# Kernel optimization log

Hardware: AMD Instinct MI355X
Metric: run time of the kernel (lower is better)

## Reference

```python
import jax, jax.numpy as jnp
import numpy as np

OUTPUT_DIM = 512
INPUT_DIM = 64
BATCH = 131072


def setup_inputs() -> dict:
    key = jax.random.key(0)
    k1, k2, k3, k4 = jax.random.split(key, 4)
    D = INPUT_DIM + OUTPUT_DIM
    X = jax.random.normal(k1, (BATCH, OUTPUT_DIM), dtype=jnp.float32)
    c = jax.random.normal(k2, (BATCH, INPUT_DIM), dtype=jnp.float32)
    PA = jax.random.normal(k3, (OUTPUT_DIM, D), dtype=jnp.float32) * 0.05
    PB = jax.random.normal(k4, (OUTPUT_DIM, D), dtype=jnp.float32) * 0.05
    return {"X": X, "c": c, "PA": PA, "PB": PB}


def reference(X, c, PA, PB):
    # x = cat(c, X) : [B, D] with D = INPUT_DIM + OUTPUT_DIM
    x = jnp.concatenate([c, X], axis=1)
    D = INPUT_DIM + OUTPUT_DIM
    mask = (jnp.arange(D)[None, :] < (INPUT_DIM + jnp.arange(OUTPUT_DIM))[:, None]).astype(x.dtype)
    A = x @ (PA * mask).T  # [B, OUTPUT_DIM], A[:, i] = pa[i] @ x[:, :INPUT_DIM+i]
    Bv = x @ (PB * mask).T  # [B, OUTPUT_DIM]
    z = X * jnp.exp(A) + Bv  # [B, OUTPUT_DIM]
    log_det = jnp.sum(A, axis=1)  # [B]
    return z, log_det
```

## Files before the change

### kernel.cpp

```cpp
#include <hip/hip_runtime.h>
#include <hip/hip_bf16.h>
#include <stdint.h>

#define N_OUT 512
#define N_IN 64
#define D_TOT 576
#define BM 64
#define ROW_BYTES (D_TOT * 2)
#define NWAVES 8

typedef __attribute__((ext_vector_type(8))) short short8_t;
typedef __attribute__((ext_vector_type(4))) float f32x4;
typedef unsigned short u16;

__device__ __forceinline__ u16 f2bf(float f) {
    __hip_bfloat16 h = __float2bfloat16(f);
    return *reinterpret_cast<u16*>(&h);
}
__device__ __forceinline__ float bf2f(u16 u) {
    union { uint32_t u; float f; } v;
    v.u = ((uint32_t)u) << 16;
    return v.f;
}

__global__ void prep_weights_kernel(const float* __restrict__ PA,
                                    const float* __restrict__ PB,
                                    u16* __restrict__ WA,
                                    u16* __restrict__ WB) {
    const int col = blockIdx.x;
    const int lim = N_IN + col;
    const float* pa = PA + (size_t)col * D_TOT;
    const float* pb = PB + (size_t)col * D_TOT;
    for (int k = threadIdx.x; k < D_TOT; k += blockDim.x) {
        int kk = k >> 5, lg = (k >> 3) & 3, j = k & 7;
        size_t dst = ((size_t)(kk * 4 + lg) * N_OUT + col) * 8 + j;
        bool valid = (k < lim);
        WA[dst] = valid ? f2bf(pa[k]) : (u16)0;
        WB[dst] = valid ? f2bf(pb[k]) : (u16)0;
    }
}

__global__ __launch_bounds__(512, 2)
void maf_main_kernel(const float* __restrict__ X,
                     const float* __restrict__ Cc,
                     const u16* __restrict__ WA,
                     const u16* __restrict__ WB,
                     float* __restrict__ Z,
                     float* __restrict__ LD) {
    extern __shared__ char smem[];
    char* xt = smem;
    float* ldsum = (float*)(smem + BM * ROW_BYTES);

    const int tid = threadIdx.x;
    const int r0 = blockIdx.x * BM;

    {
        int row = tid >> 3, cc = tid & 7;
        const float* src = Cc + (size_t)(r0 + row) * N_IN + cc * 8;
        f32x4 v0 = *(const f32x4*)src;
        f32x4 v1 = *(const f32x4*)(src + 4);
        short8_t p;
        p[0] = (short)f2bf(v0[0]); p[1] = (short)f2bf(v0[1]);
        p[2] = (short)f2bf(v0[2]); p[3] = (short)f2bf(v0[3]);
        p[4] = (short)f2bf(v1[0]); p[5] = (short)f2bf(v1[1]);
        p[6] = (short)f2bf(v1[2]); p[7] = (short)f2bf(v1[3]);
        int addr = (row * ROW_BYTES + cc * 16) ^ ((row & 7) << 4);
        *(short8_t*)(xt + addr) = p;
    }
    #pragma unroll
    for (int i = 0; i < 8; ++i) {
        int id = tid + i * 512;
        int row = id >> 6, xc = id & 63;
        const float* src = X + (size_t)(r0 + row) * N_OUT + xc * 8;
        f32x4 v0 = *(const f32x4*)src;
        f32x4 v1 = *(const f32x4*)(src + 4);
        short8_t p;
        p[0] = (short)f2bf(v0[0]); p[1] = (short)f2bf(v0[1]);
        p[2] = (short)f2bf(v0[2]); p[3] = (short)f2bf(v0[3]);
        p[4] = (short)f2bf(v1[0]); p[5] = (short)f2bf(v1[1]);
        p[6] = (short)f2bf(v1[2]); p[7] = (short)f2bf(v1[3]);
        int addr = (row * ROW_BYTES + (8 + xc) * 16) ^ ((row & 7) << 4);
        *(short8_t*)(xt + addr) = p;
    }
    __syncthreads();

    const int wid = tid >> 6;
    const int lane = tid & 63;
    const int lr = lane & 15;
    const int lg = lane >> 4;

    float part[4][4];
    #pragma unroll
    for (int m = 0; m < 4; ++m)
        #pragma unroll
        for (int j = 0; j < 4; ++j) part[m][j] = 0.0f;

    const int groups[2] = { wid, 15 - wid };

    #pragma unroll
    for (int gi = 0; gi < 2; ++gi) {
        const int g = groups[gi];
        const int c0 = g << 5;
        const int ksteps = 3 + g;

        f32x4 accA[4][2], accB[4][2];
        #pragma unroll
        for (int m = 0; m < 4; ++m)
            #pragma unroll
            for (int n = 0; n < 2; ++n) {
                accA[m][n] = (f32x4)(0.0f);
                accB[m][n] = (f32x4)(0.0f);
            }

        #pragma unroll 3
        for (int kk = 0; kk < ksteps; ++kk) {
            const int kb = kk * 64 + lg * 16;
            short8_t a[4];
            #pragma unroll
            for (int m = 0; m < 4; ++m) {
                int row = (m << 4) + lr;
                int addr = (row * ROW_BYTES + kb) ^ ((row & 7) << 4);
                a[m] = *(const short8_t*)(xt + addr);
            }
            short8_t ba[2], bb[2];
            const size_t wbase = (size_t)((kk << 2) + lg) * N_OUT + c0 + lr;
            #pragma unroll
            for (int n = 0; n < 2; ++n) {
                size_t off = (wbase + (n << 4)) * 8;
                ba[n] = *(const short8_t*)(WA + off);
                bb[n] = *(const short8_t*)(WB + off);
            }
            #pragma unroll
            for (int m = 0; m < 4; ++m) {
                #pragma unroll
                for (int n = 0; n < 2; ++n) {
                    accA[m][n] = __builtin_amdgcn_mfma_f32_16x16x32_bf16(a[m], ba[n], accA[m][n], 0, 0, 0);
                    accB[m][n] = __builtin_amdgcn_mfma_f32_16x16x32_bf16(a[m], bb[n], accB[m][n], 0, 0, 0);
                }
            }
        }

        #pragma unroll
        for (int m = 0; m < 4; ++m) {
            #pragma unroll
            for (int n = 0; n < 2; ++n) {
                int col = c0 + (n << 4) + lr;
                #pragma unroll
                for (int j = 0; j < 4; ++j) {
                    int row = (m << 4) + (lg << 2) + j;
                    float Av = accA[m][n][j];
                    float Bv = accB[m][n][j];
                    int xaddr = (row * ROW_BYTES + (N_IN + col) * 2) ^ ((row & 7) << 4);
                    float Xf = bf2f(*(const u16*)(xt + xaddr));
                    Z[(size_t)(r0 + row) * N_OUT + col] = Xf * __expf(Av) + Bv;
                    part[m][j] += Av;
                }
            }
        }
    }

    #pragma unroll
    for (int m = 0; m < 4; ++m) {
        #pragma unroll
        for (int j = 0; j < 4; ++j) {
            float v = part[m][j];
            v += __shfl_xor(v, 1);
            v += __shfl_xor(v, 2);
            v += __shfl_xor(v, 4);
            v += __shfl_xor(v, 8);
            if (lr == 0) ldsum[(wid << 6) + (m << 4) + (lg << 2) + j] = v;
        }
    }
    __syncthreads();
    if (tid < 64) {
        float s = 0.0f;
        #pragma unroll
        for (int w = 0; w < NWAVES; ++w) s += ldsum[(w << 6) + tid];
        LD[(size_t)r0 + tid] = s;
    }
}

extern "C" void kernel_launch(void* const* d_in, const int* in_sizes, int n_in,
                              void* d_out, int out_size, void* d_ws, size_t ws_size,
                              hipStream_t stream) {
    const float* X  = (const float*)d_in[0];
    const float* Cc = (const float*)d_in[1];
    const float* PA = (const float*)d_in[2];
    const float* PB = (const float*)d_in[3];

    u16* WA = (u16*)d_ws;
    u16* WB = WA + (size_t)N_OUT * D_TOT;

    float* Z  = (float*)d_out;
    const size_t batch = (size_t)in_sizes[0] / N_OUT;
    float* LD = Z + batch * N_OUT;

    prep_weights_kernel<<<N_OUT, 256, 0, stream>>>(PA, PB, WA, WB);

    const size_t lds_bytes = (size_t)BM * ROW_BYTES + NWAVES * 64 * sizeof(float);
    (void)hipFuncSetAttribute((const void*)maf_main_kernel,
                              hipFuncAttributeMaxDynamicSharedMemorySize,
                              (int)lds_bytes);
    const int grid = (int)(batch / BM);
    maf_main_kernel<<<grid, 512, lds_bytes, stream>>>(X, Cc, WA, WB, Z, LD);
}
```

Baseline: 234.3 us.

## Split output columns across blocks and pipeline weights and activations through LDS

Each row block is now split across two workgroups by output-column half, so a block only walks the K range its causal mask needs. Weight tiles are double-buffered in LDS via global_load_lds, and activation slices are streamed in per k-step alongside the MFMAs. Before, each wave read its weights directly from global memory and all activations were loaded before any compute. Partial log-det sums go to a workspace and are merged by an extra small kernel. The cost is a barrier every k-step, a 141 KB LDS footprint that allows only one block per CU, reading X twice across the two column halves, and one more launch.

```diff
diff --git a/kernel.cpp b/kernel.cpp
--- a/kernel.cpp
+++ b/kernel.cpp
@@ -6,10 +6,17 @@
 #define N_IN 64
 #define D_TOT 576
 #define BM 64
+#define BN 256
 #define ROW_BYTES (D_TOT * 2)
-#define NWAVES 8
+#define BATCH 131072
+
+#define WOFF 0
+#define XOFF 65536
+#define SOFF 139264
+#define LDS_TOTAL 141312
 
 typedef __attribute__((ext_vector_type(8))) short short8_t;
+typedef __attribute__((ext_vector_type(4))) short short4_t;
 typedef __attribute__((ext_vector_type(4))) float f32x4;
 typedef unsigned short u16;
 
@@ -40,125 +47,170 @@
     }
 }
 
-__global__ __launch_bounds__(512, 2)
+__global__ void ld_merge_kernel(const float* __restrict__ PS,
+                                float* __restrict__ LD) {
+    int i = blockIdx.x * 256 + threadIdx.x;
+    LD[i] = PS[i] + PS[BATCH + i];
+}
+
+__global__ __launch_bounds__(512)
 void maf_main_kernel(const float* __restrict__ X,
                      const float* __restrict__ Cc,
                      const u16* __restrict__ WA,
                      const u16* __restrict__ WB,
                      float* __restrict__ Z,
-                     float* __restrict__ LD) {
+                     float* __restrict__ PS) {
     extern __shared__ char smem[];
-    char* xt = smem;
-    float* ldsum = (float*)(smem + BM * ROW_BYTES);
+    char* wlds = smem + WOFF;
+    char* xt   = smem + XOFF;
+    float* ldsum = (float*)(smem + SOFF);
 
     const int tid = threadIdx.x;
-    const int r0 = blockIdx.x * BM;
-
-    {
-        int row = tid >> 3, cc = tid & 7;
-        const float* src = Cc + (size_t)(r0 + row) * N_IN + cc * 8;
-        f32x4 v0 = *(const f32x4*)src;
-        f32x4 v1 = *(const f32x4*)(src + 4);
-        short8_t p;
-        p[0] = (short)f2bf(v0[0]); p[1] = (short)f2bf(v0[1]);
-        p[2] = (short)f2bf(v0[2]); p[3] = (short)f2bf(v0[3]);
-        p[4] = (short)f2bf(v1[0]); p[5] = (short)f2bf(v1[1]);
-        p[6] = (short)f2bf(v1[2]); p[7] = (short)f2bf(v1[3]);
-        int addr = (row * ROW_BYTES + cc * 16) ^ ((row & 7) << 4);
-        *(short8_t*)(xt + addr) = p;
-    }
-    #pragma unroll
-    for (int i = 0; i < 8; ++i) {
-        int id = tid + i * 512;
-        int row = id >> 6, xc = id & 63;
-        const float* src = X + (size_t)(r0 + row) * N_OUT + xc * 8;
-        f32x4 v0 = *(const f32x4*)src;
-        f32x4 v1 = *(const f32x4*)(src + 4);
-        short8_t p;
-        p[0] = (short)f2bf(v0[0]); p[1] = (short)f2bf(v0[1]);
-        p[2] = (short)f2bf(v0[2]); p[3] = (short)f2bf(v0[3]);
-        p[4] = (short)f2bf(v1[0]); p[5] = (short)f2bf(v1[1]);
-        p[6] = (short)f2bf(v1[2]); p[7] = (short)f2bf(v1[3]);
-        int addr = (row * ROW_BYTES + (8 + xc) * 16) ^ ((row & 7) << 4);
-        *(short8_t*)(xt + addr) = p;
-    }
-    __syncthreads();
-
-    const int wid = tid >> 6;
+    const int bid = blockIdx.x;
+    const int cb  = bid & 1;
+    const int rb  = bid >> 1;
+    const int r0  = rb * BM;
+    const int cbase = cb * BN;
+
+    const int wid  = tid >> 6;
     const int lane = tid & 63;
     const int lr = lane & 15;
     const int lg = lane >> 4;
 
-    float part[4][4];
-    #pragma unroll
-    for (int m = 0; m < 4; ++m)
-        #pragma unroll
-        for (int j = 0; j < 4; ++j) part[m][j] = 0.0f;
-
-    const int groups[2] = { wid, 15 - wid };
-
-    #pragma unroll
-    for (int gi = 0; gi < 2; ++gi) {
-        const int g = groups[gi];
-        const int c0 = g << 5;
-        const int ksteps = 3 + g;
-
-        f32x4 accA[4][2], accB[4][2];
-        #pragma unroll
-        for (int m = 0; m < 4; ++m)
+    const int T0 = (cb << 4) + wid;
+    const int T1 = (cb << 4) + 15 - wid;
+    const int ks0 = (111 + 16 * T0) >> 5;
+    const int ks1 = (111 + 16 * T1) >> 5;
+    const int kmax = 10 + 8 * cb;
+
+    const int xrow = tid >> 3, xq = tid & 7;
+
+    {
+        int kb = xq * 4;
+        f32x4 v = __builtin_nontemporal_load(
+            (const f32x4*)(Cc + (size_t)(r0 + xrow) * N_IN + kb));
+        short4_t p;
+        p[0] = (short)f2bf(v[0]); p[1] = (short)f2bf(v[1]);
+        p[2] = (short)f2bf(v[2]); p[3] = (short)f2bf(v[3]);
+        int addr = (xrow * ROW_BYTES + kb * 2) ^ ((xrow & 7) << 4);
+        *(short4_t*)(xt + addr) = p;
+    }
+    #pragma unroll
+    for (int i = 0; i < 4; ++i) {
+        int f = i * 512 + tid;
+        int mat = f >> 10, q = f & 1023;
+        int lg2 = q >> 8, col = q & 255;
+        const u16* g = (mat ? WB : WA) + ((size_t)lg2 * N_OUT + cbase + col) * 8;
+        char* l = wlds + f * 16;
+        __builtin_amdgcn_global_load_lds(
+            (const __attribute__((address_space(1))) uint32_t*)g,
+            (__attribute__((address_space(3))) uint32_t*)l, 16, 0, 0);
+    }
+    __syncthreads();
+
+    f32x4 aE0[4], aV0[4], aE1[4], aV1[4];
+    #pragma unroll
+    for (int m = 0; m < 4; ++m) {
+        aE0[m] = (f32x4)(0.0f); aV0[m] = (f32x4)(0.0f);
+        aE1[m] = (f32x4)(0.0f); aV1[m] = (f32x4)(0.0f);
+    }
+
+    const int cl0 = ((T0 & 15) << 4) + lr;
+    const int cl1 = ((T1 & 15) << 4) + lr;
+
+    int buf = 0;
+    for (int kk = 0; kk < kmax; ++kk) {
+        const int s = kk + 1;
+        f32x4 xv;
+        if (s < kmax) {
+            int kb = s * 32 + xq * 4;
+            const float* src = (s < 2)
+                ? (Cc + (size_t)(r0 + xrow) * N_IN + kb)
+                : (X + (size_t)(r0 + xrow) * N_OUT + (kb - 64));
+            xv = __builtin_nontemporal_load((const f32x4*)src);
+        }
+        if (s < kmax) {
             #pragma unroll
-            for (int n = 0; n < 2; ++n) {
-                accA[m][n] = (f32x4)(0.0f);
-                accB[m][n] = (f32x4)(0.0f);
-            }
-
-        #pragma unroll 3
-        for (int kk = 0; kk < ksteps; ++kk) {
-            const int kb = kk * 64 + lg * 16;
-            short8_t a[4];
+            for (int i = 0; i < 4; ++i) {
+                int f = i * 512 + tid;
+                int mat = f >> 10, q = f & 1023;
+                int lg2 = q >> 8, col = q & 255;
+                const u16* g = (mat ? WB : WA)
+                    + ((size_t)((s << 2) + lg2) * N_OUT + cbase + col) * 8;
+                char* l = wlds + (buf ^ 1) * 32768 + f * 16;
+                __builtin_amdgcn_global_load_lds(
+                    (const __attribute__((address_space(1))) uint32_t*)g,
+                    (__attribute__((address_space(3))) uint32_t*)l, 16, 0, 0);
+            }
+        }
+        const char* wb_ = wlds + buf * 32768;
+        short8_t a[4];
+        #pragma unroll
+        for (int m = 0; m < 4; ++m) {
+            int row = (m << 4) + lr;
+            int addr = (row * ROW_BYTES + kk * 64 + lg * 16) ^ ((row & 7) << 4);
+            a[m] = *(const short8_t*)(xt + addr);
+        }
+        if (kk < ks0) {
+            short8_t we = *(const short8_t*)(wb_ + ((lg << 8) + cl0) * 16);
+            short8_t wv = *(const short8_t*)(wb_ + 16384 + ((lg << 8) + cl0) * 16);
             #pragma unroll
             for (int m = 0; m < 4; ++m) {
-                int row = (m << 4) + lr;
-                int addr = (row * ROW_BYTES + kb) ^ ((row & 7) << 4);
-                a[m] = *(const short8_t*)(xt + addr);
-            }
-            short8_t ba[2], bb[2];
-            const size_t wbase = (size_t)((kk << 2) + lg) * N_OUT + c0 + lr;
-            #pragma unroll
-            for (int n = 0; n < 2; ++n) {
-                size_t off = (wbase + (n << 4)) * 8;
-                ba[n] = *(const short8_t*)(WA + off);
-                bb[n] = *(const short8_t*)(WB + off);
-            }
+                aE0[m] = __builtin_amdgcn_mfma_f32_16x16x32_bf16(a[m], we, aE0[m], 0, 0, 0);
+                aV0[m] = __builtin_amdgcn_mfma_f32_16x16x32_bf16(a[m], wv, aV0[m], 0, 0, 0);
+            }
+        }
+        if (kk < ks1) {
+            short8_t we = *(const short8_t*)(wb_ + ((lg << 8) + cl1) * 16);
+            short8_t wv = *(const short8_t*)(wb_ + 16384 + ((lg << 8) + cl1) * 16);
             #pragma unroll
             for (int m = 0; m < 4; ++m) {
-                #pragma unroll
-                for (int n = 0; n < 2; ++n) {
-                    accA[m][n] = __builtin_amdgcn_mfma_f32_16x16x32_bf16(a[m], ba[n], accA[m][n], 0, 0, 0);
-                    accB[m][n] = __builtin_amdgcn_mfma_f32_16x16x32_bf16(a[m], bb[n], accB[m][n], 0, 0, 0);
-                }
-            }
-        }
-
-        #pragma unroll
-        for (int m = 0; m < 4; ++m) {
-            #pragma unroll
-            for (int n = 0; n < 2; ++n) {
-                int col = c0 + (n << 4) + lr;
-                #pragma unroll
-                for (int j = 0; j < 4; ++j) {
-                    int row = (m << 4) + (lg << 2) + j;
-                    float Av = accA[m][n][j];
-                    float Bv = accB[m][n][j];
-                    int xaddr = (row * ROW_BYTES + (N_IN + col) * 2) ^ ((row & 7) << 4);
-                    float Xf = bf2f(*(const u16*)(xt + xaddr));
-                    Z[(size_t)(r0 + row) * N_OUT + col] = Xf * __expf(Av) + Bv;
-                    part[m][j] += Av;
-                }
-            }
-        }
-    }
-
+                aE1[m] = __builtin_amdgcn_mfma_f32_16x16x32_bf16(a[m], we, aE1[m], 0, 0, 0);
+                aV1[m] = __builtin_amdgcn_mfma_f32_16x16x32_bf16(a[m], wv, aV1[m], 0, 0, 0);
+            }
+        }
+        if (s < kmax) {
+            int kb = s * 32 + xq * 4;
+            short4_t p;
+            p[0] = (short)f2bf(xv[0]); p[1] = (short)f2bf(xv[1]);
+            p[2] = (short)f2bf(xv[2]); p[3] = (short)f2bf(xv[3]);
+            int addr = (xrow * ROW_BYTES + kb * 2) ^ ((xrow & 7) << 4);
+            *(short4_t*)(xt + addr) = p;
+        }
+        __syncthreads();
+        buf ^= 1;
+    }
+
+    float part[4][4];
+    #pragma unroll
+    for (int m = 0; m < 4; ++m)
+        #pragma unroll
+        for (int j = 0; j < 4; ++j) part[m][j] = 0.0f;
+
+    const int gcol0 = (T0 << 4) + lr;
+    const int gcol1 = (T1 << 4) + lr;
+    #pragma unroll
+    for (int m = 0; m < 4; ++m) {
+        #pragma unroll
+        for (int j = 0; j < 4; ++j) {
+            int row = (m << 4) + (lg << 2) + j;
+            int swz = (row & 7) << 4;
+            {
+                float Av = aE0[m][j], Bv = aV0[m][j];
+                int xb = (row * ROW_BYTES + (N_IN + gcol0) * 2) ^ swz;
+                float Xf = bf2f(*(const u16*)(xt + xb));
+                Z[(size_t)(r0 + row) * N_OUT + gcol0] = Xf * __expf(Av) + Bv;
+                part[m][j] += Av;
+            }
+            {
+                float Av = aE1[m][j], Bv = aV1[m][j];
+                int xb = (row * ROW_BYTES + (N_IN + gcol1) * 2) ^ swz;
+                float Xf = bf2f(*(const u16*)(xt + xb));
+                Z[(size_t)(r0 + row) * N_OUT + gcol1] = Xf * __expf(Av) + Bv;
+                part[m][j] += Av;
+            }
+        }
+    }
     #pragma unroll
     for (int m = 0; m < 4; ++m) {
         #pragma unroll
@@ -172,11 +224,11 @@
         }
     }
     __syncthreads();
-    if (tid < 64) {
+    if (tid < BM) {
         float s = 0.0f;
         #pragma unroll
-        for (int w = 0; w < NWAVES; ++w) s += ldsum[(w << 6) + tid];
-        LD[(size_t)r0 + tid] = s;
+        for (int w = 0; w < 8; ++w) s += ldsum[(w << 6) + tid];
+        PS[(size_t)cb * BATCH + r0 + tid] = s;
     }
 }
 
@@ -190,17 +242,18 @@
 
     u16* WA = (u16*)d_ws;
     u16* WB = WA + (size_t)N_OUT * D_TOT;
+    float* PS = (float*)((char*)d_ws + 2 * (size_t)N_OUT * D_TOT * 2);
 
     float* Z  = (float*)d_out;
-    const size_t batch = (size_t)in_sizes[0] / N_OUT;
-    float* LD = Z + batch * N_OUT;
+    float* LD = Z + (size_t)BATCH * N_OUT;
 
     prep_weights_kernel<<<N_OUT, 256, 0, stream>>>(PA, PB, WA, WB);
 
-    const size_t lds_bytes = (size_t)BM * ROW_BYTES + NWAVES * 64 * sizeof(float);
     (void)hipFuncSetAttribute((const void*)maf_main_kernel,
                               hipFuncAttributeMaxDynamicSharedMemorySize,
-                              (int)lds_bytes);
-    const int grid = (int)(batch / BM);
-    maf_main_kernel<<<grid, 512, lds_bytes, stream>>>(X, Cc, WA, WB, Z, LD);
-}
+                              LDS_TOTAL);
+    const int grid = 2 * (BATCH / BM);
+    maf_main_kernel<<<grid, 512, LDS_TOTAL, stream>>>(X, Cc, WA, WB, Z, PS);
+
+    ld_merge_kernel<<<BATCH / 256, 256, 0, stream>>>(PS, LD);
+}
```

Result: slower. 377.5 us (+61.2%).
